# Kernel tuning notes

Hardware: AMD Instinct MI355X
Metric: run time of the kernel (lower is better)

Reference implementation:

```python
import jax, jax.numpy as jnp
import numpy as np

# Irreps spec: 32x0e (dim 1, with bias) + 16x1o (dim 3) + 8x2e (dim 5)
# x: [B, n_channels_in, 120] where 120 = 32*1 + 16*3 + 8*5

B = 1024
N_IN = 256
N_OUT = 256


def setup_inputs() -> dict:
    key = jax.random.key(0)
    k_x, k0, k1, k2 = jax.random.split(key, 4)
    std = 1.0 / np.sqrt(N_IN)
    x = jax.random.normal(k_x, (B, N_IN, 120), dtype=jnp.float32)
    W0 = jax.random.normal(k0, (32, N_OUT, N_IN), dtype=jnp.float32) * std
    W1 = jax.random.normal(k1, (16, N_OUT, N_IN), dtype=jnp.float32) * std
    W2 = jax.random.normal(k2, (8, N_OUT, N_IN), dtype=jnp.float32) * std
    b0 = jnp.zeros((32, N_OUT), dtype=jnp.float32)
    return {"x": x, "W0": W0, "W1": W1, "W2": W2, "b0": b0}


def reference(x, W0, W1, W2, b0):
    # Grouped form of the original per-multiplicity loop. Slices of the last
    # axis are consecutive per (irrep, multiplicity), so reshaping a group of
    # `mul` copies of an irrep of dim `d` to [..., n_in, mul, d] and doing one
    # batched einsum reproduces the original concatenation order exactly.
    groups = [(W0, 1, b0), (W1, 3, None), (W2, 5, None)]  # (weights[mul,o,i], irrep dim, bias[mul,o] or None)
    outs = []
    start = 0
    for W, d, b in groups:
        mul = W.shape[0]
        width = mul * d
        xs = x[..., start:start + width].reshape(*x.shape[:-1], mul, d)  # [..., n_in, mul, d]
        y = jnp.einsum('moi,...imd->...omd', W, xs)  # [..., n_out, mul, d]
        if b is not None:  # only l=0 irreps get a bias, broadcast over d (=1)
            y = y + b.T[:, :, None]  # [n_out, mul, 1]
        outs.append(y.reshape(*y.shape[:-2], width))  # [..., n_out, mul*d]
        start += width
    return jnp.concatenate(outs, axis=-1)  # [..., n_out, 120]
```

## Files before the change

kernel.cpp:

```cpp
#include <hip/hip_runtime.h>

typedef __attribute__((ext_vector_type(8))) short bf16x8;
typedef __attribute__((ext_vector_type(4))) float f32x4;
typedef __attribute__((ext_vector_type(8))) unsigned short u16x8;

#define DEVINL __device__ __forceinline__
#define AS1 __attribute__((address_space(1)))
#define AS3 __attribute__((address_space(3)))

constexpr int NI = 256;
constexpr int NO = 256;
constexpr int NC = 120;
constexpr int BROW = NC * NI;
constexpr int WELEMS = 56 * NO * NI;
constexpr size_t XT_ELEMS = (size_t)NC * 1024 * NI;

DEVINL ushort f2bf(float x) {
  unsigned u = __float_as_uint(x);
  u += 0x7FFFu + ((u >> 16) & 1u);
  return (ushort)(u >> 16);
}
DEVINL float bf2f(ushort v) { return __uint_as_float((unsigned)v << 16); }

__global__ __launch_bounds__(256) void prep_w(const float* __restrict__ w0,
                                              const float* __restrict__ w1,
                                              const float* __restrict__ w2,
                                              ushort* __restrict__ wb) {
  const int m = blockIdx.x >> 5;
  const int kc = blockIdx.x & 31;
  const int o = threadIdx.x;
  const float* src;
  if (m < 32)      src = w0 + ((size_t)(m * NO + o)) * NI;
  else if (m < 48) src = w1 + ((size_t)((m - 32) * NO + o)) * NI;
  else             src = w2 + ((size_t)((m - 48) * NO + o)) * NI;
  src += kc * 8;
  float4 a = *reinterpret_cast<const float4*>(src);
  float4 b = *reinterpret_cast<const float4*>(src + 4);
  u16x8 p = { f2bf(a.x), f2bf(a.y), f2bf(a.z), f2bf(a.w),
              f2bf(b.x), f2bf(b.y), f2bf(b.z), f2bf(b.w) };
  *reinterpret_cast<u16x8*>(wb + ((size_t)(blockIdx.x * 256 + o)) * 8) = p;
}

__global__ __launch_bounds__(256) void xpose(const float* __restrict__ x,
                                             ushort* __restrict__ xt) {
  __shared__ float tl[64 * 121];
  const int bid = blockIdx.x;
  const int b = bid >> 2, iq = bid & 3;
  const int t = threadIdx.x;
  const float* xb = x + (size_t)b * BROW + (size_t)iq * 64 * NC;
#pragma unroll
  for (int j = 0; j < 15; ++j) {
    const int e = (j * 256 + t) * 2;
    float2 v = *reinterpret_cast<const float2*>(xb + e);
    const int i = e / 120, c = e % 120;
    tl[i * 121 + c] = v.x;
    tl[i * 121 + c + 1] = v.y;
  }
  __syncthreads();
  ushort* dst = xt + (size_t)b * BROW + iq * 64;
#pragma unroll
  for (int q = 0; q < 4; ++q) {
    const int chunk = q * 256 + t;
    if (chunk < 960) {
      const int c = chunk >> 3, ich = chunk & 7;
      u16x8 p;
#pragma unroll
      for (int k = 0; k < 8; ++k) p[k] = f2bf(tl[(ich * 8 + k) * 121 + c]);
      *reinterpret_cast<u16x8*>(dst + (size_t)c * NI + ich * 8) = p;
    }
  }
}

__global__ __launch_bounds__(512, 4) void e3mix9(const ushort* __restrict__ xt,
                                                 const ushort* __restrict__ wb,
                                                 const float* __restrict__ bias0,
                                                 float* __restrict__ out) {
  __shared__ ushort xs[2 * 16384];
  const int bid = blockIdx.x;
  const int oq = bid & 3;
  const int rest = bid >> 2;
  const int ct = rest % 15;
  const int bt = rest / 15;
  const int c0 = ct * 8, bg = bt * 32, og = oq * 64;

  const int tid = threadIdx.x, lane = tid & 63, w = tid >> 6;
  const int rb = lane & 15, rg = lane >> 4;
  const int c = c0 + w;
  const int m = c < 32 ? c : (c < 80 ? 32 + (c - 32) / 3 : 48 + (c - 80) / 5);

  const int lr = lane >> 3;
  const ushort* gsrc = xt + (size_t)(bg + lr) * BROW + (size_t)c * NI
                          + ((lane & 7) ^ lr) * 8;

  f32x4 acc[2][4];
#pragma unroll
  for (int i = 0; i < 2; ++i)
#pragma unroll
    for (int j = 0; j < 4; ++j) acc[i][j] = (f32x4)0.0f;

#define STAGE9(BUF, S)                                                         \
  do {                                                                         \
    __builtin_amdgcn_global_load_lds(                                          \
        (const AS1 void*)(gsrc + (size_t)(S) * 64 + (size_t)0 * 8 * BROW),     \
        (AS3 void*)(xs + (BUF) * 16384 + w * 2048 + 0 * 512), 16, 0, 0);       \
    __builtin_amdgcn_global_load_lds(                                          \
        (const AS1 void*)(gsrc + (size_t)(S) * 64 + (size_t)1 * 8 * BROW),     \
        (AS3 void*)(xs + (BUF) * 16384 + w * 2048 + 1 * 512), 16, 0, 0);       \
    __builtin_amdgcn_global_load_lds(                                          \
        (const AS1 void*)(gsrc + (size_t)(S) * 64 + (size_t)2 * 8 * BROW),     \
        (AS3 void*)(xs + (BUF) * 16384 + w * 2048 + 2 * 512), 16, 0, 0);       \
    __builtin_amdgcn_global_load_lds(                                          \
        (const AS1 void*)(gsrc + (size_t)(S) * 64 + (size_t)3 * 8 * BROW),     \
        (AS3 void*)(xs + (BUF) * 16384 + w * 2048 + 3 * 512), 16, 0, 0);       \
  } while (0)

  STAGE9(0, 0);
  __syncthreads();

#pragma unroll 1
  for (int s = 0; s < 4; ++s) {
    if (s < 3) STAGE9((s + 1) & 1, s + 1);
    const ushort* xb = xs + (s & 1) * 16384 + w * 2048;
#pragma unroll
    for (int kh = 0; kh < 2; ++kh) {
      bf16x8 a[2], wf[4];
#pragma unroll
      for (int fb = 0; fb < 2; ++fb)
        a[fb] = *reinterpret_cast<const bf16x8*>(
            xb + (fb * 16 + rb) * 64 + (((kh * 4 + rg) ^ (rb & 7)) * 8));
#pragma unroll
      for (int fo = 0; fo < 4; ++fo)
        wf[fo] = *reinterpret_cast<const bf16x8*>(
            wb + ((size_t)((m * 32 + s * 8 + kh * 4 + rg) * NO
                           + og + fo * 16 + rb)) * 8);
#pragma unroll
      for (int fb = 0; fb < 2; ++fb)
#pragma unroll
        for (int fo = 0; fo < 4; ++fo)
          acc[fb][fo] = __builtin_amdgcn_mfma_f32_16x16x32_bf16(a[fb], wf[fo],
                                                                acc[fb][fo], 0, 0, 0);
    }
    __syncthreads();
  }
#undef STAGE9

  if (c0 < 32) {
#pragma unroll
    for (int fo = 0; fo < 4; ++fo) {
      const float bv = bias0[c * NO + og + fo * 16 + rb];
#pragma unroll
      for (int fb = 0; fb < 2; ++fb) acc[fb][fo] += bv;
    }
  }

#pragma unroll
  for (int fb = 0; fb < 2; ++fb)
#pragma unroll
    for (int r = 0; r < 4; ++r)
#pragma unroll
      for (int fo = 0; fo < 4; ++fo)
        xs[(fb * 16 + rg * 4 + r) * 520 + (fo * 16 + rb) * 8 + w] =
            f2bf(acc[fb][fo][r]);
  __syncthreads();
#pragma unroll
  for (int i = 0; i < 4; ++i) {
    const int g = i * 512 + tid;
    const int bp = g >> 6, o = g & 63;
    u16x8 v = *reinterpret_cast<const u16x8*>(xs + bp * 520 + o * 8);
    float4 lo = make_float4(bf2f(v[0]), bf2f(v[1]), bf2f(v[2]), bf2f(v[3]));
    float4 hi = make_float4(bf2f(v[4]), bf2f(v[5]), bf2f(v[6]), bf2f(v[7]));
    float* dst = out + ((size_t)(bg + bp) * NO + og + o) * NC + c0;
    *reinterpret_cast<float4*>(dst) = lo;
    *reinterpret_cast<float4*>(dst + 4) = hi;
  }
}

__global__ __launch_bounds__(512, 4) void e3mix2f(const float* __restrict__ x,
                                                  const ushort* __restrict__ wb,
                                                  const float* __restrict__ bias0,
                                                  float* __restrict__ out) {
  __shared__ ushort xs[8 * 16 * 64];
  const int bid = blockIdx.x;
  const int ct = bid % 15, bt = bid / 15;
  const int c0 = ct * 8, bg = bt * 16;
  const int t = threadIdx.x, lane = t & 63, wid = t >> 6;
  const int sb = lane >> 2, sp = lane & 3;
  const int rb = lane & 15, rg = lane >> 4;
  const int oc = wid * 16 + rb;
  const int srow = (wid * 16 + sb) * 64;
  const int sk0 = (sp * 16) ^ ((sb & 7) << 3);
  const int sk1 = (sp * 16 + 8) ^ ((sb & 7) << 3);

  f32x4 acc[8][2];
#pragma unroll
  for (int i = 0; i < 8; ++i) { acc[i][0] = (f32x4)0.0f; acc[i][1] = (f32x4)0.0f; }
  bf16x8 w00 = {}, w01 = {}, w10 = {}, w11 = {};

#pragma unroll 1
  for (int s = 0; s < 4; ++s) {
    if (s) __syncthreads();
    u16x8 v0, v1;
    const float* src = x + (size_t)(bg + sb) * (NI * NC)
                         + (size_t)(s * 64 + sp * 16) * NC + (c0 + wid);
#pragma unroll
    for (int jj = 0; jj < 8; ++jj) v0[jj] = f2bf(src[jj * NC]);
#pragma unroll
    for (int jj = 0; jj < 8; ++jj) v1[jj] = f2bf(src[(8 + jj) * NC]);
    *reinterpret_cast<u16x8*>(&xs[srow + sk0]) = v0;
    *reinterpret_cast<u16x8*>(&xs[srow + sk1]) = v1;
    __syncthreads();

    int mprev = -1;
#pragma unroll
    for (int cc = 0; cc < 8; ++cc) {
      const int c = c0 + cc;
      const int m = c < 32 ? c : (c < 80 ? 32 + (c - 32) / 3 : 48 + (c - 80) / 5);
      if (m != mprev) {
        const ushort* wp = wb + ((size_t)((m * 32 + s * 8 + rg) * NO + oc)) * 8;
        w00 = *reinterpret_cast<const bf16x8*>(wp);
        w10 = *reinterpret_cast<const bf16x8*>(wp + (size_t)4 * NO * 8);
        w01 = *reinterpret_cast<const bf16x8*>(wp + 128 * 8);
        w11 = *reinterpret_cast<const bf16x8*>(wp + (size_t)4 * NO * 8 + 128 * 8);
        mprev = m;
      }
      const ushort* xp = xs + (cc * 16 + rb) * 64;
      const int sz = (rb & 7) << 3;
      bf16x8 a0 = *reinterpret_cast<const bf16x8*>(xp + ((rg * 8) ^ sz));
      bf16x8 a1 = *reinterpret_cast<const bf16x8*>(xp + ((32 + rg * 8) ^ sz));
      acc[cc][0] = __builtin_amdgcn_mfma_f32_16x16x32_bf16(a0, w00, acc[cc][0], 0, 0, 0);
      acc[cc][0] = __builtin_amdgcn_mfma_f32_16x16x32_bf16(a1, w10, acc[cc][0], 0, 0, 0);
      acc[cc][1] = __builtin_amdgcn_mfma_f32_16x16x32_bf16(a0, w01, acc[cc][1], 0, 0, 0);
      acc[cc][1] = __builtin_amdgcn_mfma_f32_16x16x32_bf16(a1, w11, acc[cc][1], 0, 0, 0);
    }
  }

  if (c0 < 32) {
#pragma unroll
    for (int cc = 0; cc < 8; ++cc) {
      acc[cc][0] += bias0[(c0 + cc) * NO + oc];
      acc[cc][1] += bias0[(c0 + cc) * NO + oc + 128];
    }
  }

  const int br0 = bg + rg * 4;
#pragma unroll
  for (int of = 0; of < 2; ++of)
#pragma unroll
    for (int r = 0; r < 4; ++r) {
      float4 va = make_float4(acc[0][of][r], acc[1][of][r], acc[2][of][r], acc[3][of][r]);
      float4 vb = make_float4(acc[4][of][r], acc[5][of][r], acc[6][of][r], acc[7][of][r]);
      float* dst = out + ((size_t)(br0 + r) * NO + oc + of * 128) * NC + c0;
      *reinterpret_cast<float4*>(dst) = va;
      *reinterpret_cast<float4*>(dst + 4) = vb;
    }
}

extern "C" void kernel_launch(void* const* d_in, const int* in_sizes, int n_in,
                              void* d_out, int out_size, void* d_ws, size_t ws_size,
                              hipStream_t stream) {
  const float* x  = (const float*)d_in[0];
  const float* w0 = (const float*)d_in[1];
  const float* w1 = (const float*)d_in[2];
  const float* w2 = (const float*)d_in[3];
  const float* b0 = (const float*)d_in[4];
  float* out = (float*)d_out;
  ushort* wb = (ushort*)d_ws;
  ushort* xt = wb + WELEMS;

  prep_w<<<56 * 32, 256, 0, stream>>>(w0, w1, w2, wb);
  const bool big = ws_size >= (size_t)2 * (WELEMS + XT_ELEMS);
  if (big) {
    xpose<<<4096, 256, 0, stream>>>(x, xt);
    e3mix9<<<1920, 512, 0, stream>>>(xt, wb, b0, out);
  } else {
    e3mix2f<<<960, 512, 0, stream>>>(x, wb, b0, out);
  }
}
```

Before: 161.9 us.

## Store transposed x channel-major and stage K in smaller double-buffered chunks

The transpose kernel now writes bf16 x as [channel][batch][n_in] planes instead of [batch][channel][n_in], so each wave's staged rows for one channel are contiguous across the batch tile. The GEMM kernel stages 32-element K chunks over 8 steps with a halved LDS footprint and a 4-way swizzle, and reorders the block index so channel tiles are outermost. This aims to improve global-load locality and occupancy through lower LDS use, at the cost of more barriers and smaller per-step work. The epilogue's reuse of xs (520-stride rows) may now exceed the reduced 16640-element buffer, though it appears to fit.

```diff
diff --git a/kernel.cpp b/kernel.cpp
--- a/kernel.cpp
+++ b/kernel.cpp
@@ -12,6 +12,7 @@
 constexpr int NO = 256;
 constexpr int NC = 120;
 constexpr int BROW = NC * NI;
+constexpr int CPLANE = 1024 * NI;
 constexpr int WELEMS = 56 * NO * NI;
 constexpr size_t XT_ELEMS = (size_t)NC * 1024 * NI;
 
@@ -57,7 +58,7 @@
     tl[i * 121 + c + 1] = v.y;
   }
   __syncthreads();
-  ushort* dst = xt + (size_t)b * BROW + iq * 64;
+  ushort* dst = xt + (size_t)b * NI + iq * 64;
 #pragma unroll
   for (int q = 0; q < 4; ++q) {
     const int chunk = q * 256 + t;
@@ -66,21 +67,20 @@
       u16x8 p;
 #pragma unroll
       for (int k = 0; k < 8; ++k) p[k] = f2bf(tl[(ich * 8 + k) * 121 + c]);
-      *reinterpret_cast<u16x8*>(dst + (size_t)c * NI + ich * 8) = p;
-    }
-  }
-}
-
-__global__ __launch_bounds__(512, 4) void e3mix9(const ushort* __restrict__ xt,
+      *reinterpret_cast<u16x8*>(dst + (size_t)c * CPLANE + ich * 8) = p;
+    }
+  }
+}
+
+__global__ __launch_bounds__(512, 4) void e3mixA(const ushort* __restrict__ xt,
                                                  const ushort* __restrict__ wb,
                                                  const float* __restrict__ bias0,
                                                  float* __restrict__ out) {
-  __shared__ ushort xs[2 * 16384];
+  __shared__ ushort xs[16640];
   const int bid = blockIdx.x;
+  const int ct = bid >> 7;
+  const int bt = (bid & 127) >> 2;
   const int oq = bid & 3;
-  const int rest = bid >> 2;
-  const int ct = rest % 15;
-  const int bt = rest / 15;
   const int c0 = ct * 8, bg = bt * 32, og = oq * 64;
 
   const int tid = threadIdx.x, lane = tid & 63, w = tid >> 6;
@@ -88,9 +88,8 @@
   const int c = c0 + w;
   const int m = c < 32 ? c : (c < 80 ? 32 + (c - 32) / 3 : 48 + (c - 80) / 5);
 
-  const int lr = lane >> 3;
-  const ushort* gsrc = xt + (size_t)(bg + lr) * BROW + (size_t)c * NI
-                          + ((lane & 7) ^ lr) * 8;
+  const ushort* gsrc = xt + (size_t)c * CPLANE + (size_t)(bg + (lane >> 2)) * NI
+                          + (((lane & 3) ^ ((lane >> 2) & 3)) * 8);
 
   f32x4 acc[2][4];
 #pragma unroll
@@ -98,51 +97,39 @@
 #pragma unroll
     for (int j = 0; j < 4; ++j) acc[i][j] = (f32x4)0.0f;
 
-#define STAGE9(BUF, S)                                                         \
+#define STAGEA(BUF, S)                                                         \
   do {                                                                         \
-    __builtin_amdgcn_global_load_lds(                                          \
-        (const AS1 void*)(gsrc + (size_t)(S) * 64 + (size_t)0 * 8 * BROW),     \
-        (AS3 void*)(xs + (BUF) * 16384 + w * 2048 + 0 * 512), 16, 0, 0);       \
-    __builtin_amdgcn_global_load_lds(                                          \
-        (const AS1 void*)(gsrc + (size_t)(S) * 64 + (size_t)1 * 8 * BROW),     \
-        (AS3 void*)(xs + (BUF) * 16384 + w * 2048 + 1 * 512), 16, 0, 0);       \
-    __builtin_amdgcn_global_load_lds(                                          \
-        (const AS1 void*)(gsrc + (size_t)(S) * 64 + (size_t)2 * 8 * BROW),     \
-        (AS3 void*)(xs + (BUF) * 16384 + w * 2048 + 2 * 512), 16, 0, 0);       \
-    __builtin_amdgcn_global_load_lds(                                          \
-        (const AS1 void*)(gsrc + (size_t)(S) * 64 + (size_t)3 * 8 * BROW),     \
-        (AS3 void*)(xs + (BUF) * 16384 + w * 2048 + 3 * 512), 16, 0, 0);       \
+    __builtin_amdgcn_global_load_lds((const AS1 void*)(gsrc + (S) * 32),       \
+        (AS3 void*)(xs + (BUF) * 8192 + w * 1024), 16, 0, 0);                  \
+    __builtin_amdgcn_global_load_lds((const AS1 void*)(gsrc + (S) * 32 + 16 * NI), \
+        (AS3 void*)(xs + (BUF) * 8192 + w * 1024 + 512), 16, 0, 0);            \
   } while (0)
 
-  STAGE9(0, 0);
+  STAGEA(0, 0);
   __syncthreads();
 
 #pragma unroll 1
-  for (int s = 0; s < 4; ++s) {
-    if (s < 3) STAGE9((s + 1) & 1, s + 1);
-    const ushort* xb = xs + (s & 1) * 16384 + w * 2048;
-#pragma unroll
-    for (int kh = 0; kh < 2; ++kh) {
-      bf16x8 a[2], wf[4];
-#pragma unroll
-      for (int fb = 0; fb < 2; ++fb)
-        a[fb] = *reinterpret_cast<const bf16x8*>(
-            xb + (fb * 16 + rb) * 64 + (((kh * 4 + rg) ^ (rb & 7)) * 8));
+  for (int s = 0; s < 8; ++s) {
+    if (s < 7) STAGEA((s + 1) & 1, s + 1);
+    const ushort* xb = xs + (s & 1) * 8192 + w * 1024;
+    bf16x8 a[2], wf[4];
+#pragma unroll
+    for (int fb = 0; fb < 2; ++fb)
+      a[fb] = *reinterpret_cast<const bf16x8*>(
+          xb + fb * 512 + rb * 32 + ((rg ^ (rb & 3)) * 8));
+#pragma unroll
+    for (int fo = 0; fo < 4; ++fo)
+      wf[fo] = *reinterpret_cast<const bf16x8*>(
+          wb + ((size_t)((m * 32 + s * 4 + rg) * NO + og + fo * 16 + rb)) * 8);
+#pragma unroll
+    for (int fb = 0; fb < 2; ++fb)
 #pragma unroll
       for (int fo = 0; fo < 4; ++fo)
-        wf[fo] = *reinterpret_cast<const bf16x8*>(
-            wb + ((size_t)((m * 32 + s * 8 + kh * 4 + rg) * NO
-                           + og + fo * 16 + rb)) * 8);
-#pragma unroll
-      for (int fb = 0; fb < 2; ++fb)
-#pragma unroll
-        for (int fo = 0; fo < 4; ++fo)
-          acc[fb][fo] = __builtin_amdgcn_mfma_f32_16x16x32_bf16(a[fb], wf[fo],
-                                                                acc[fb][fo], 0, 0, 0);
-    }
+        acc[fb][fo] = __builtin_amdgcn_mfma_f32_16x16x32_bf16(a[fb], wf[fo],
+                                                              acc[fb][fo], 0, 0, 0);
     __syncthreads();
   }
-#undef STAGE9
+#undef STAGEA
 
   if (c0 < 32) {
 #pragma unroll
@@ -271,7 +258,7 @@
   const bool big = ws_size >= (size_t)2 * (WELEMS + XT_ELEMS);
   if (big) {
     xpose<<<4096, 256, 0, stream>>>(x, xt);
-    e3mix9<<<1920, 512, 0, stream>>>(xt, wb, b0, out);
+    e3mixA<<<1920, 512, 0, stream>>>(xt, wb, b0, out);
   } else {
     e3mix2f<<<960, 512, 0, stream>>>(x, wb, b0, out);
   }
```

After: 157.9 us. -2.5%, faster.
